# Performance work log

Measured on AMD Instinct MI355X. Metric: run time of the kernel, lower is better.

Reference implementation:

```python
import jax, jax.numpy as jnp
import numpy as np

N, M, D = 131072, 128, 128

def setup_inputs() -> dict:
    key = jax.random.key(0)
    k1, k2, k3 = jax.random.split(key, 3)
    X = jax.random.normal(k1, (N, D), dtype=jnp.float32)
    r = jax.random.uniform(k2, (N, M), dtype=jnp.float32)
    mus = jax.random.normal(k3, (M, D), dtype=jnp.float32)
    return {"X": X, "r": r, "mus": mus}

def reference(X, r, mus):
    # Squared pairwise L2 distances without materializing [N, M, D]:
    x2 = jnp.sum(X * X, axis=1)            # [N]
    mu2 = jnp.sum(mus * mus, axis=1)       # [M]
    cross = X @ mus.T                      # [N, M]
    dist2 = jnp.maximum(x2[:, None] + mu2[None, :] - 2.0 * cross, 0.0)
    loss = jnp.sum(r * dist2) / X.shape[0]
    return loss
```

## Files before the change

### kernel.cpp

```cpp
#include <hip/hip_runtime.h>
#include <hip/hip_bf16.h>


typedef __attribute__((ext_vector_type(8)))  short  short8;
typedef __attribute__((ext_vector_type(16))) float  float16v;

#if defined(__has_builtin)
#if __has_builtin(__builtin_amdgcn_cvt_pk_bf16_f32)
#define HAVE_PK_BF16 1
#endif
#endif

__device__ __forceinline__ unsigned int pk_bf16(float x, float y) {
#ifdef HAVE_PK_BF16
    typedef __attribute__((ext_vector_type(2))) __bf16 bf16x2;
    bf16x2 p = __builtin_amdgcn_cvt_pk_bf16_f32(x, y);
    return __builtin_bit_cast(unsigned int, p);
#else
    unsigned int ux = __float_as_uint(x);
    unsigned int uy = __float_as_uint(y);
    ux += 0x7fffu + ((ux >> 16) & 1u);
    uy += 0x7fffu + ((uy >> 16) & 1u);
    return (ux >> 16) | (uy & 0xffff0000u);
#endif
}

__global__ void final_reduce_kernel(const float* ws, float* out) {
    const int lane = threadIdx.x;
    float t = ws[lane];
    #pragma unroll
    for (int off = 32; off > 0; off >>= 1) t += __shfl_down(t, off);
    if (lane == 0) out[0] = t * (1.0f / 131072.0f);
}

__global__ __launch_bounds__(256)
void build_afrag_kernel(const float* __restrict__ mus, uint4* __restrict__ afrag,
                        float* __restrict__ ws)
{
    const int g = blockIdx.x * 256 + threadIdx.x;
    if (blockIdx.x == 0 && threadIdx.x < 64) ws[threadIdx.x] = 0.0f;

    const int dt   = g >> 9;
    const int rem  = g & 511;
    const int ks   = rem >> 6;
    const int lane = rem & 63;
    const int dp   = dt * 32 + (lane & 31);
    const int m0   = ks * 16 + (lane >> 5) * 8;

    float v[8];
    if (dp < 128) {
        #pragma unroll
        for (int e = 0; e < 8; ++e)
            v[e] = mus[(size_t)(m0 + e) * 128 + dp];
    } else if (dp == 128) {
        #pragma unroll
        for (int e = 0; e < 8; ++e) {
            const float4* row = (const float4*)(mus + (size_t)(m0 + e) * 128);
            float a = 0.0f;
            #pragma unroll 8
            for (int d4 = 0; d4 < 32; ++d4) {
                const float4 t = row[d4];
                a += t.x*t.x + t.y*t.y + t.z*t.z + t.w*t.w;
            }
            v[e] = a;
        }
    } else if (dp == 129) {
        #pragma unroll
        for (int e = 0; e < 8; ++e) v[e] = 1.0f;
    } else {
        #pragma unroll
        for (int e = 0; e < 8; ++e) v[e] = 0.0f;
    }

    uint4 u;
    u.x = pk_bf16(v[0], v[1]);
    u.y = pk_bf16(v[2], v[3]);
    u.z = pk_bf16(v[4], v[5]);
    u.w = pk_bf16(v[6], v[7]);
    afrag[g] = u;
}

__global__ __launch_bounds__(256, 4)
void isoloss_kernel(const float* __restrict__ X,
                    const float* __restrict__ r,
                    const uint4* __restrict__ afrag,
                    float* __restrict__ ws)
{
    const int tid  = threadIdx.x;
    const int w    = blockIdx.x * 4 + (tid >> 6);
    const int lane = tid & 63;
    const int col  = lane & 31;
    const int half = lane >> 5;

    const size_t i = (size_t)w * 32 + col;
    const float* rrow_p = r + i * 128;
    const float* xrow_p = X + i * 128;

    short8 bfrag[8];
    #pragma unroll
    for (int ks = 0; ks < 8; ++ks) {
        const float4 a = *(const float4*)(rrow_p + ks * 16 + half * 8);
        const float4 b = *(const float4*)(rrow_p + ks * 16 + half * 8 + 4);
        union { short8 s8; uint4 u4; } u;
        u.u4.x = pk_bf16(a.x, a.y);
        u.u4.y = pk_bf16(a.z, a.w);
        u.u4.z = pk_bf16(b.x, b.y);
        u.u4.w = pk_bf16(b.z, b.w);
        bfrag[ks] = u.s8;
    }

    float dotp = 0.0f, x2p = 0.0f, rmu2v = 0.0f, rrowv = 0.0f;

    #pragma unroll
    for (int dt = 0; dt < 5; ++dt) {
        short8 af[8];
        #pragma unroll
        for (int ks = 0; ks < 8; ++ks)
            af[ks] = ((const short8*)afrag)[(dt * 8 + ks) * 64 + lane];

        float16v acc = {};
        #pragma unroll
        for (int ks = 0; ks < 8; ++ks)
            acc = __builtin_amdgcn_mfma_f32_32x32x16_bf16(af[ks], bfrag[ks], acc, 0, 0, 0);

        if (dt < 4) {
            float4 xq[4];
            #pragma unroll
            for (int q = 0; q < 4; ++q)
                xq[q] = *(const float4*)(xrow_p + dt * 32 + q * 8 + half * 4);
            #pragma unroll
            for (int reg = 0; reg < 16; ++reg) {
                const float x = xq[reg >> 2][reg & 3];
                dotp += x * acc[reg];
                x2p  += x * x;
            }
        } else {
            rmu2v = acc[0];
            rrowv = acc[1];
        }
    }

    const float x2i = x2p + __shfl_xor(x2p, 32);
    float s = x2i * rrowv + rmu2v - 2.0f * dotp;

    #pragma unroll
    for (int off = 32; off > 0; off >>= 1) s += __shfl_down(s, off);
    if (lane == 0) atomicAdd(&ws[blockIdx.x & 63], s);
}

extern "C" void kernel_launch(void* const* d_in, const int* in_sizes, int n_in,
                              void* d_out, int out_size, void* d_ws, size_t ws_size,
                              hipStream_t stream) {
    const float* X   = (const float*)d_in[0];
    const float* r   = (const float*)d_in[1];
    const float* mus = (const float*)d_in[2];
    float* out = (float*)d_out;
    float* ws  = (float*)d_ws;
    uint4* afrag = (uint4*)((char*)d_ws + 256);

    build_afrag_kernel<<<10, 256, 0, stream>>>(mus, afrag, ws);
    isoloss_kernel<<<1024, 256, 0, stream>>>(X, r, afrag, ws);
    final_reduce_kernel<<<1, 64, 0, stream>>>(ws, out);
}
```

Before: 183.3 us.

## Switch to 16x16x32 bf16 MFMA tiles with smaller per-wave row blocks

Replaces the 32x32x16 MFMA tiling with 16x16x32, so each wave handles 16 rows and the afrag layout is rebuilt to match, with less padding in the augmented mu dimension. Grid size doubles and launch bounds request 8 blocks per CU, lowering register pressure to raise occupancy and hide the latency of the strided loads of r and X. The trade-off is more waves, an extra shuffle stage for the x2 reduction, and a different memory access pattern per instruction.

```diff
diff --git a/kernel.cpp b/kernel.cpp
--- a/kernel.cpp
+++ b/kernel.cpp
@@ -2,8 +2,8 @@
 #include <hip/hip_bf16.h>
 
 
-typedef __attribute__((ext_vector_type(8)))  short  short8;
-typedef __attribute__((ext_vector_type(16))) float  float16v;
+typedef __attribute__((ext_vector_type(8))) short  short8;
+typedef __attribute__((ext_vector_type(4))) float  float4v;
 
 #if defined(__has_builtin)
 #if __has_builtin(__builtin_amdgcn_cvt_pk_bf16_f32)
@@ -40,12 +40,11 @@
     const int g = blockIdx.x * 256 + threadIdx.x;
     if (blockIdx.x == 0 && threadIdx.x < 64) ws[threadIdx.x] = 0.0f;
 
-    const int dt   = g >> 9;
-    const int rem  = g & 511;
-    const int ks   = rem >> 6;
-    const int lane = rem & 63;
-    const int dp   = dt * 32 + (lane & 31);
-    const int m0   = ks * 16 + (lane >> 5) * 8;
+    const int dt   = g >> 8;
+    const int ks   = (g >> 6) & 3;
+    const int lane = g & 63;
+    const int dp   = dt * 16 + (lane & 15);
+    const int m0   = ks * 32 + (lane >> 4) * 8;
 
     float v[8];
     if (dp < 128) {
@@ -80,27 +79,27 @@
     afrag[g] = u;
 }
 
-__global__ __launch_bounds__(256, 4)
+__global__ __launch_bounds__(256, 8)
 void isoloss_kernel(const float* __restrict__ X,
                     const float* __restrict__ r,
                     const uint4* __restrict__ afrag,
                     float* __restrict__ ws)
 {
     const int tid  = threadIdx.x;
-    const int w    = blockIdx.x * 4 + (tid >> 6);
+    const int wv   = blockIdx.x * 4 + (tid >> 6);
     const int lane = tid & 63;
-    const int col  = lane & 31;
-    const int half = lane >> 5;
+    const int li   = lane & 15;
+    const int kg   = lane >> 4;
 
-    const size_t i = (size_t)w * 32 + col;
-    const float* rrow_p = r + i * 128;
-    const float* xrow_p = X + i * 128;
+    const size_t i = (size_t)wv * 16 + li;
+    const float* rrow_p = r + i * 128 + kg * 8;
+    const float* xrow_p = X + i * 128 + kg * 4;
 
-    short8 bfrag[8];
+    short8 bfrag[4];
     #pragma unroll
-    for (int ks = 0; ks < 8; ++ks) {
-        const float4 a = *(const float4*)(rrow_p + ks * 16 + half * 8);
-        const float4 b = *(const float4*)(rrow_p + ks * 16 + half * 8 + 4);
+    for (int ks = 0; ks < 4; ++ks) {
+        const float4 a = *(const float4*)(rrow_p + ks * 32);
+        const float4 b = *(const float4*)(rrow_p + ks * 32 + 4);
         union { short8 s8; uint4 u4; } u;
         u.u4.x = pk_bf16(a.x, a.y);
         u.u4.y = pk_bf16(a.z, a.w);
@@ -112,36 +111,32 @@
     float dotp = 0.0f, x2p = 0.0f, rmu2v = 0.0f, rrowv = 0.0f;
 
     #pragma unroll
-    for (int dt = 0; dt < 5; ++dt) {
-        short8 af[8];
+    for (int dt = 0; dt < 9; ++dt) {
+        short8 af[4];
         #pragma unroll
-        for (int ks = 0; ks < 8; ++ks)
-            af[ks] = ((const short8*)afrag)[(dt * 8 + ks) * 64 + lane];
+        for (int ks = 0; ks < 4; ++ks)
+            af[ks] = ((const short8*)afrag)[(dt * 4 + ks) * 64 + lane];
 
-        float16v acc = {};
+        float4v acc = {};
         #pragma unroll
-        for (int ks = 0; ks < 8; ++ks)
-            acc = __builtin_amdgcn_mfma_f32_32x32x16_bf16(af[ks], bfrag[ks], acc, 0, 0, 0);
+        for (int ks = 0; ks < 4; ++ks)
+            acc = __builtin_amdgcn_mfma_f32_16x16x32_bf16(af[ks], bfrag[ks], acc, 0, 0, 0);
 
-        if (dt < 4) {
-            float4 xq[4];
-            #pragma unroll
-            for (int q = 0; q < 4; ++q)
-                xq[q] = *(const float4*)(xrow_p + dt * 32 + q * 8 + half * 4);
-            #pragma unroll
-            for (int reg = 0; reg < 16; ++reg) {
-                const float x = xq[reg >> 2][reg & 3];
-                dotp += x * acc[reg];
-                x2p  += x * x;
-            }
+        if (dt < 8) {
+            const float4 xq = *(const float4*)(xrow_p + dt * 16);
+            dotp += xq.x*acc[0] + xq.y*acc[1] + xq.z*acc[2] + xq.w*acc[3];
+            x2p  += xq.x*xq.x + xq.y*xq.y + xq.z*xq.z + xq.w*xq.w;
         } else {
-            rmu2v = acc[0];
-            rrowv = acc[1];
+            rmu2v = (kg == 0) ? acc[0] : 0.0f;
+            rrowv = (kg == 0) ? acc[1] : 0.0f;
         }
     }
 
-    const float x2i = x2p + __shfl_xor(x2p, 32);
-    float s = x2i * rrowv + rmu2v - 2.0f * dotp;
+    float x2i = x2p;
+    x2i += __shfl_xor(x2i, 16);
+    x2i += __shfl_xor(x2i, 32);
+
+    float s = fmaf(-2.0f, dotp, fmaf(x2i, rrowv, rmu2v));
 
     #pragma unroll
     for (int off = 32; off > 0; off >>= 1) s += __shfl_down(s, off);
@@ -158,7 +153,7 @@
     float* ws  = (float*)d_ws;
     uint4* afrag = (uint4*)((char*)d_ws + 256);
 
-    build_afrag_kernel<<<10, 256, 0, stream>>>(mus, afrag, ws);
-    isoloss_kernel<<<1024, 256, 0, stream>>>(X, r, afrag, ws);
+    build_afrag_kernel<<<9, 256, 0, stream>>>(mus, afrag, ws);
+    isoloss_kernel<<<2048, 256, 0, stream>>>(X, r, afrag, ws);
     final_reduce_kernel<<<1, 64, 0, stream>>>(ws, out);
 }
```

New measurement: 194.0 us. 1.06x slower.
